# Kernel tuning notes

Measured on AMD Instinct MI355X. Metric: run time of the kernel, lower is better.

## Reference

```python
import jax, jax.numpy as jnp
import numpy as np

N, P, Q, T, J, B, H = 262144, 64, 64, 2048, 512, 8, 64


def setup_inputs() -> dict:
    key = jax.random.key(0)
    ks = jax.random.split(key, 11)
    sH = 1.0 / np.sqrt(H).astype(np.float32)
    return {
        "idx": jax.random.randint(ks[0], (B,), 0, J),
        "seg_ids": jnp.sort(jax.random.randint(ks[1], (N,), 0, T)),
        "K": jax.random.normal(ks[2], (N, P), jnp.float32) * 0.1,
        "V": jax.random.normal(ks[3], (N, Q), jnp.float32),
        "S": jax.random.normal(ks[4], (P, J), jnp.float32) * 0.1,
        "W_ih": jax.random.normal(ks[5], (3 * H, Q), jnp.float32) * sH,
        "W_hh": jax.random.normal(ks[6], (3 * H, H), jnp.float32) * sH,
        "b_ih": jax.random.normal(ks[7], (3 * H,), jnp.float32) * sH,
        "b_hh": jax.random.normal(ks[8], (3 * H,), jnp.float32) * sH,
        "w_out": jax.random.normal(ks[9], (1, H), jnp.float32) * sH,
        "b_out": jax.random.normal(ks[10], (1,), jnp.float32) * sH,
    }


def reference(idx, seg_ids, K, V, S, W_ih, W_hh, b_ih, b_hh, w_out, b_out):
    # W[:, b] = K @ S[:, idx[b]]  -> [N, B]
    w = K @ S[:, idx]
    # ragged per-segment softmax over the N axis (segments = date windows)
    m = jax.ops.segment_max(w, seg_ids, num_segments=T)          # [T, B]
    e = jnp.exp(w - m[seg_ids])                                  # [N, B]
    denom = jax.ops.segment_sum(e, seg_ids, num_segments=T)     # [T, B]
    alpha = e / denom[seg_ids]                                   # [N, B]
    # weighted aggregation of V rows per segment: M[t, b] = sum_u alpha_u * V_u
    M = jax.ops.segment_sum(alpha[:, :, None] * V[:, None, :],
                            seg_ids, num_segments=T)             # [T, B, Q]
    X = jnp.transpose(M, (1, 0, 2))                              # [B, T, Q]

    # PyTorch GRU (gate order r,z,n). Faithful to the original bug: GRU was
    # built without batch_first=True, so axis 0 (B) is time, axis 1 (T) is batch.
    def step(h, x_t):  # x_t: [T, Q], h: [T, H]
        gi = x_t @ W_ih.T + b_ih                                 # [T, 3H]
        gh = h @ W_hh.T + b_hh                                   # [T, 3H]
        i_r, i_z, i_n = jnp.split(gi, 3, axis=1)
        h_r, h_z, h_n = jnp.split(gh, 3, axis=1)
        r = jax.nn.sigmoid(i_r + h_r)
        z = jax.nn.sigmoid(i_z + h_z)
        n = jnp.tanh(i_n + r * h_n)
        h_new = (1.0 - z) * n + z * h
        return h_new, h_new

    h0 = jnp.zeros((T, H), X.dtype)
    _, hs = jax.lax.scan(step, h0, X)                            # [B, T, H]
    preds = hs @ w_out.T + b_out                                 # [B, T, 1]
    return preds
```

## Files before the change

kernel.cpp:

```cpp
#include <hip/hip_runtime.h>
#include <math.h>

#define NN 262144
#define PP 64
#define QQ 64
#define TT 2048
#define JJ 512
#define BB 8
#define HH 64

__device__ __forceinline__ float lane_bcast(float v, int l) {
  return __int_as_float(__builtin_amdgcn_readlane(__float_as_int(v), l));
}

__global__ __launch_bounds__(256) void k_wp(const float* __restrict__ Kmat,
                                            const int* __restrict__ idx,
                                            const float* __restrict__ S,
                                            const int* __restrict__ seg_ids,
                                            float* __restrict__ ew,
                                            int* __restrict__ seg_start) {
  int tid = threadIdx.x;
  int gtid = blockIdx.x * 256 + tid;
  if (gtid <= TT) {
    int lo = 0, hi = NN;
    while (lo < hi) {
      int mid = (lo + hi) >> 1;
      if (seg_ids[mid] < gtid) lo = mid + 1; else hi = mid;
    }
    seg_start[gtid] = lo;
  }
  __shared__ __align__(16) float s_lds[BB * PP];
  for (int i = tid; i < BB * PP; i += 256) {
    int p = i >> 3, b = i & 7;
    s_lds[b * PP + p] = S[p * JJ + idx[b]];
  }
  __syncthreads();
  int n = blockIdx.x * 64 + (tid >> 2);
  int sub = tid & 3;
  const float4* Kp = reinterpret_cast<const float4*>(Kmat + (size_t)n * PP + sub * 16);
  float4 kq[4];
#pragma unroll
  for (int j = 0; j < 4; ++j) kq[j] = Kp[j];
  float acc[8];
#pragma unroll
  for (int b = 0; b < 8; ++b) acc[b] = 0.f;
#pragma unroll
  for (int j4 = 0; j4 < 4; ++j4) {
    float4 kk = kq[j4];
#pragma unroll
    for (int b = 0; b < 8; ++b) {
      const float4 sv = *reinterpret_cast<const float4*>(&s_lds[b * PP + sub * 16 + j4 * 4]);
      acc[b] += kk.x * sv.x + kk.y * sv.y + kk.z * sv.z + kk.w * sv.w;
    }
  }
#pragma unroll
  for (int b = 0; b < 8; ++b) {
    acc[b] += __shfl_xor(acc[b], 1);
    acc[b] += __shfl_xor(acc[b], 2);
  }
  float ox = (sub == 0) ? acc[0] : (sub == 1) ? acc[2] : (sub == 2) ? acc[4] : acc[6];
  float oy = (sub == 0) ? acc[1] : (sub == 1) ? acc[3] : (sub == 2) ? acc[5] : acc[7];
  reinterpret_cast<float2*>(ew + (size_t)n * 8)[sub] =
      make_float2(__expf(ox), __expf(oy));
}

__global__ __launch_bounds__(512) void k_segS(const float* __restrict__ ew,
                                              const float* __restrict__ V,
                                              const int* __restrict__ seg_start,
                                              float* __restrict__ M) {
  __shared__ __align__(16) float accred[8][8][64];
  __shared__ float reds[8][8];
  int tid = threadIdx.x;
  int t = blockIdx.x;
  int lane = tid & 63;
  int w = __builtin_amdgcn_readfirstlane(tid >> 6);
  int s = seg_start[t], e = seg_start[t + 1];
  int len = e - s;
  int chunk = (len + 7) >> 3;
  int b0 = __builtin_amdgcn_readfirstlane(s + w * chunk);
  int b1 = b0 + chunk; if (b1 > e) b1 = e;
  b1 = __builtin_amdgcn_readfirstlane(b1);
  if (b1 < b0) b1 = b0;

  float acc[8], se[8];
#pragma unroll
  for (int b = 0; b < 8; ++b) { acc[b] = 0.f; se[b] = 0.f; }

  int r = b0;
  for (; r + 4 <= b1; r += 4) {
#pragma unroll
    for (int u = 0; u < 4; ++u) {
      const float* er = ew + (size_t)(r + u) * 8;
      float e0 = er[0], e1 = er[1], e2 = er[2], e3 = er[3];
      float e4 = er[4], e5 = er[5], e6 = er[6], e7 = er[7];
      float v = V[(size_t)(r + u) * QQ + lane];
      acc[0] += e0 * v; acc[1] += e1 * v; acc[2] += e2 * v; acc[3] += e3 * v;
      acc[4] += e4 * v; acc[5] += e5 * v; acc[6] += e6 * v; acc[7] += e7 * v;
      se[0] += e0; se[1] += e1; se[2] += e2; se[3] += e3;
      se[4] += e4; se[5] += e5; se[6] += e6; se[7] += e7;
    }
  }
  for (; r < b1; ++r) {
    const float* er = ew + (size_t)r * 8;
    float e0 = er[0], e1 = er[1], e2 = er[2], e3 = er[3];
    float e4 = er[4], e5 = er[5], e6 = er[6], e7 = er[7];
    float v = V[(size_t)r * QQ + lane];
    acc[0] += e0 * v; acc[1] += e1 * v; acc[2] += e2 * v; acc[3] += e3 * v;
    acc[4] += e4 * v; acc[5] += e5 * v; acc[6] += e6 * v; acc[7] += e7 * v;
    se[0] += e0; se[1] += e1; se[2] += e2; se[3] += e3;
    se[4] += e4; se[5] += e5; se[6] += e6; se[7] += e7;
  }

#pragma unroll
  for (int b = 0; b < 8; ++b) accred[w][b][lane] = acc[b];
  if (lane == 0) {
#pragma unroll
    for (int b = 0; b < 8; ++b) reds[w][b] = se[b];
  }
  __syncthreads();
  {
    int o = tid;
    int b = o >> 6, q = o & 63;
    float dd = 0.f, sum = 0.f;
#pragma unroll
    for (int jj = 0; jj < 8; ++jj) { dd += reds[jj][b]; sum += accred[jj][b][q]; }
    float inv = (dd > 0.f) ? 1.f / dd : 0.f;
    M[(size_t)t * 512 + o] = sum * inv;
  }
}

__global__ __launch_bounds__(256) void k_gi(const float* __restrict__ M,
                                            const float* __restrict__ W_ih,
                                            const float* __restrict__ b_ih,
                                            float* __restrict__ GI) {
  __shared__ float Wt[64 * 193];
  int tid = threadIdx.x;
  for (int i = tid; i < 192 * 64; i += 256) {
    int g = i >> 6, k = i & 63;
    Wt[k * 193 + g] = W_ih[i];
  }
  __syncthreads();
  int lane = tid & 63, wv = tid >> 6;
  int row0 = blockIdx.x * 32 + wv * 8;
  float x[8];
#pragma unroll
  for (int rr = 0; rr < 8; ++rr) {
    int rho = row0 + rr;
    int b = rho >> 11, t = rho & 2047;
    x[rr] = M[((size_t)t * 8 + b) * 64 + lane];
  }
  float bi0 = b_ih[lane], bi1 = b_ih[64 + lane], bi2 = b_ih[128 + lane];
  float a0[8], a1[8], a2[8];
#pragma unroll
  for (int rr = 0; rr < 8; ++rr) { a0[rr] = bi0; a1[rr] = bi1; a2[rr] = bi2; }
#pragma unroll
  for (int k = 0; k < 64; ++k) {
    float w0 = Wt[k * 193 + lane];
    float w1 = Wt[k * 193 + 64 + lane];
    float w2 = Wt[k * 193 + 128 + lane];
#pragma unroll
    for (int rr = 0; rr < 8; ++rr) {
      float xk = lane_bcast(x[rr], k);
      a0[rr] += w0 * xk; a1[rr] += w1 * xk; a2[rr] += w2 * xk;
    }
  }
#pragma unroll
  for (int rr = 0; rr < 8; ++rr) {
    size_t rho = (size_t)row0 + rr;
    GI[rho * 192 + lane]       = a0[rr];
    GI[rho * 192 + 64 + lane]  = a1[rr];
    GI[rho * 192 + 128 + lane] = a2[rr];
  }
}

__global__ __launch_bounds__(256) void k_gru(const float* __restrict__ GI,
                                             const float* __restrict__ W_hh,
                                             const float* __restrict__ b_hh,
                                             const float* __restrict__ w_out,
                                             const float* __restrict__ b_out,
                                             float* __restrict__ preds) {
  __shared__ __align__(16) float Wl[192 * 68];
  int tid = threadIdx.x;
  for (int i = tid; i < 192 * 16; i += 256) {
    int g = i >> 4, c = i & 15;
    *reinterpret_cast<float4*>(&Wl[g * 68 + c * 4]) =
        *reinterpret_cast<const float4*>(W_hh + g * 64 + c * 4);
  }
  __syncthreads();
  int lane = tid & 63, wv = tid >> 6;
  int t = blockIdx.x * 4 + wv;
  float bh0 = b_hh[lane], bh1 = b_hh[64 + lane], bh2 = b_hh[128 + lane];
  float wo = w_out[lane];
  float bo = b_out[0];
  const float* w0base = &Wl[lane * 68];
  const float* w1base = &Wl[(64 + lane) * 68];
  const float* w2base = &Wl[(128 + lane) * 68];

  float gr[8], gz[8], gn[8];
#pragma unroll
  for (int b = 0; b < 8; ++b) {
    size_t base = ((size_t)b * TT + t) * 192;
    gr[b] = GI[base + lane];
    gz[b] = GI[base + 64 + lane];
    gn[b] = GI[base + 128 + lane];
  }

  float h;
  {
    float r = 1.f / (1.f + __expf(-(gr[0] + bh0)));
    float z = 1.f / (1.f + __expf(-(gz[0] + bh1)));
    float nv = tanhf(gn[0] + r * bh2);
    h = (1.f - z) * nv;
    float pv = h * wo;
#pragma unroll
    for (int off = 32; off; off >>= 1) pv += __shfl_xor(pv, off);
    if (lane == 0) preds[t] = pv + bo;
  }
#pragma unroll
  for (int b = 1; b < 8; ++b) {
    float ar = bh0, az = bh1, an = bh2;
#pragma unroll
    for (int c = 0; c < 16; ++c) {
      const float4 w0 = *reinterpret_cast<const float4*>(w0base + c * 4);
      const float4 w1 = *reinterpret_cast<const float4*>(w1base + c * 4);
      const float4 w2 = *reinterpret_cast<const float4*>(w2base + c * 4);
      float a0 = lane_bcast(h, c * 4 + 0), a1 = lane_bcast(h, c * 4 + 1);
      float a2 = lane_bcast(h, c * 4 + 2), a3 = lane_bcast(h, c * 4 + 3);
      ar += w0.x * a0 + w0.y * a1 + w0.z * a2 + w0.w * a3;
      az += w1.x * a0 + w1.y * a1 + w1.z * a2 + w1.w * a3;
      an += w2.x * a0 + w2.y * a1 + w2.z * a2 + w2.w * a3;
    }
    float r = 1.f / (1.f + __expf(-(gr[b] + ar)));
    float z = 1.f / (1.f + __expf(-(gz[b] + az)));
    float nv = tanhf(gn[b] + r * an);
    h = (1.f - z) * nv + z * h;
    float pv = h * wo;
#pragma unroll
    for (int off = 32; off; off >>= 1) pv += __shfl_xor(pv, off);
    if (lane == 0) preds[(size_t)b * TT + t] = pv + bo;
  }
}

extern "C" void kernel_launch(void* const* d_in, const int* in_sizes, int n_in,
                              void* d_out, int out_size, void* d_ws, size_t ws_size,
                              hipStream_t stream) {
  const int*   idx     = (const int*)d_in[0];
  const int*   seg_ids = (const int*)d_in[1];
  const float* Kmat    = (const float*)d_in[2];
  const float* V       = (const float*)d_in[3];
  const float* S       = (const float*)d_in[4];
  const float* W_ih    = (const float*)d_in[5];
  const float* W_hh    = (const float*)d_in[6];
  const float* b_ih    = (const float*)d_in[7];
  const float* b_hh    = (const float*)d_in[8];
  const float* w_out   = (const float*)d_in[9];
  const float* b_out   = (const float*)d_in[10];
  float* out = (float*)d_out;

  char* ws = (char*)d_ws;
  int*   seg_start = (int*)(ws + 0);
  float* ew = (float*)(ws + 8448);
  float* M  = (float*)(ws + 8397056);
  float* GI = (float*)(ws + 12591360);

  hipLaunchKernelGGL(k_wp, dim3(NN / 64), dim3(256), 0, stream,
                     Kmat, idx, S, seg_ids, ew, seg_start);
  hipLaunchKernelGGL(k_segS, dim3(TT), dim3(512), 0, stream, ew, V, seg_start, M);
  hipLaunchKernelGGL(k_gi, dim3(512), dim3(256), 0, stream, M, W_ih, b_ih, GI);
  hipLaunchKernelGGL(k_gru, dim3(512), dim3(256), 0, stream, GI, W_hh, b_hh, w_out, b_out, out);
}
```

Measured before the change: 69.79 us.

## Fuse segment aggregation with GRU input projection into one kernel

Merges the segment-softmax aggregation kernel and the W_ih input-projection kernel so each block keeps its M tile in shared memory and computes GI directly, removing the M round trip through global memory and one launch. Each of the 2048 blocks now stages the full transposed W_ih (about 48KB) into LDS, which repeats that load many times and raises shared-memory use per block, possibly lowering occupancy of the bandwidth-bound aggregation phase. The projection also loses the 8-row register blocking the old kernel had.

```diff
diff --git a/kernel.cpp b/kernel.cpp
--- a/kernel.cpp
+++ b/kernel.cpp
@@ -64,16 +64,26 @@
       make_float2(__expf(ox), __expf(oy));
 }
 
-__global__ __launch_bounds__(512) void k_segS(const float* __restrict__ ew,
-                                              const float* __restrict__ V,
-                                              const int* __restrict__ seg_start,
-                                              float* __restrict__ M) {
+__global__ __launch_bounds__(512) void k_segGI(const float* __restrict__ ew,
+                                               const float* __restrict__ V,
+                                               const int* __restrict__ seg_start,
+                                               const float* __restrict__ W_ih,
+                                               const float* __restrict__ b_ih,
+                                               float* __restrict__ GI) {
   __shared__ __align__(16) float accred[8][8][64];
   __shared__ float reds[8][8];
+  __shared__ __align__(16) float Mtile[512];
+  __shared__ float Wt[64 * 193];
   int tid = threadIdx.x;
   int t = blockIdx.x;
   int lane = tid & 63;
   int w = __builtin_amdgcn_readfirstlane(tid >> 6);
+
+  for (int i = tid; i < 192 * 64; i += 512) {
+    int g = i >> 6, k = i & 63;
+    Wt[k * 193 + g] = W_ih[i];
+  }
+
   int s = seg_start[t], e = seg_start[t + 1];
   int len = e - s;
   int chunk = (len + 7) >> 3;
@@ -125,51 +135,25 @@
 #pragma unroll
     for (int jj = 0; jj < 8; ++jj) { dd += reds[jj][b]; sum += accred[jj][b][q]; }
     float inv = (dd > 0.f) ? 1.f / dd : 0.f;
-    M[(size_t)t * 512 + o] = sum * inv;
-  }
-}
-
-__global__ __launch_bounds__(256) void k_gi(const float* __restrict__ M,
-                                            const float* __restrict__ W_ih,
-                                            const float* __restrict__ b_ih,
-                                            float* __restrict__ GI) {
-  __shared__ float Wt[64 * 193];
-  int tid = threadIdx.x;
-  for (int i = tid; i < 192 * 64; i += 256) {
-    int g = i >> 6, k = i & 63;
-    Wt[k * 193 + g] = W_ih[i];
-  }
-  __syncthreads();
-  int lane = tid & 63, wv = tid >> 6;
-  int row0 = blockIdx.x * 32 + wv * 8;
-  float x[8];
-#pragma unroll
-  for (int rr = 0; rr < 8; ++rr) {
-    int rho = row0 + rr;
-    int b = rho >> 11, t = rho & 2047;
-    x[rr] = M[((size_t)t * 8 + b) * 64 + lane];
-  }
-  float bi0 = b_ih[lane], bi1 = b_ih[64 + lane], bi2 = b_ih[128 + lane];
-  float a0[8], a1[8], a2[8];
-#pragma unroll
-  for (int rr = 0; rr < 8; ++rr) { a0[rr] = bi0; a1[rr] = bi1; a2[rr] = bi2; }
-#pragma unroll
-  for (int k = 0; k < 64; ++k) {
-    float w0 = Wt[k * 193 + lane];
-    float w1 = Wt[k * 193 + 64 + lane];
-    float w2 = Wt[k * 193 + 128 + lane];
-#pragma unroll
-    for (int rr = 0; rr < 8; ++rr) {
-      float xk = lane_bcast(x[rr], k);
-      a0[rr] += w0 * xk; a1[rr] += w1 * xk; a2[rr] += w2 * xk;
-    }
-  }
-#pragma unroll
-  for (int rr = 0; rr < 8; ++rr) {
-    size_t rho = (size_t)row0 + rr;
-    GI[rho * 192 + lane]       = a0[rr];
-    GI[rho * 192 + 64 + lane]  = a1[rr];
-    GI[rho * 192 + 128 + lane] = a2[rr];
+    Mtile[o] = sum * inv;
+  }
+  __syncthreads();
+
+  {
+    float x = Mtile[w * 64 + lane];
+    float a0 = b_ih[lane], a1 = b_ih[64 + lane], a2 = b_ih[128 + lane];
+#pragma unroll
+    for (int k = 0; k < 64; ++k) {
+      float w0 = Wt[k * 193 + lane];
+      float w1 = Wt[k * 193 + 64 + lane];
+      float w2 = Wt[k * 193 + 128 + lane];
+      float xk = lane_bcast(x, k);
+      a0 += w0 * xk; a1 += w1 * xk; a2 += w2 * xk;
+    }
+    size_t rho = (size_t)w * TT + t;
+    GI[rho * 192 + lane]       = a0;
+    GI[rho * 192 + 64 + lane]  = a1;
+    GI[rho * 192 + 128 + lane] = a2;
   }
 }
 
@@ -260,12 +244,12 @@
   char* ws = (char*)d_ws;
   int*   seg_start = (int*)(ws + 0);
   float* ew = (float*)(ws + 8448);
-  float* M  = (float*)(ws + 8397056);
-  float* GI = (float*)(ws + 12591360);
+  float* GI = (float*)(ws + 8397056);
 
   hipLaunchKernelGGL(k_wp, dim3(NN / 64), dim3(256), 0, stream,
                      Kmat, idx, S, seg_ids, ew, seg_start);
-  hipLaunchKernelGGL(k_segS, dim3(TT), dim3(512), 0, stream, ew, V, seg_start, M);
-  hipLaunchKernelGGL(k_gi, dim3(512), dim3(256), 0, stream, M, W_ih, b_ih, GI);
-  hipLaunchKernelGGL(k_gru, dim3(512), dim3(256), 0, stream, GI, W_hh, b_hh, w_out, b_out, out);
-}
+  hipLaunchKernelGGL(k_segGI, dim3(TT), dim3(512), 0, stream,
+                     ew, V, seg_start, W_ih, b_ih, GI);
+  hipLaunchKernelGGL(k_gru, dim3(512), dim3(256), 0, stream,
+                     GI, W_hh, b_hh, w_out, b_out, out);
+}
```

New measurement: 73.84 us. +5.8%, slower.
